# Performance work log

Hardware: AMD Instinct MI355X
Metric: run time of the kernel (lower is better)

Reference implementation:

```python
import jax, jax.numpy as jnp
import numpy as np

N_CLASSES_FG = 20  # n_classes - 1

def _norm(t, axis=1):
    # F.normalize(t, dim=axis, eps=1e-10)
    n = jnp.linalg.norm(t, axis=axis, keepdims=True)
    return t / jnp.maximum(n, 1e-10)

def setup_inputs() -> dict:
    key = jax.random.key(0)
    ks = jax.random.split(key, 6)
    B, C, H, W = 8, 512, 80, 80
    N, Hr, Wr = 100, 40, 40
    return {
        "code_C": jax.random.normal(ks[0], (B, C, H, W), jnp.float32),
        "code_BG": jax.random.normal(ks[1], (B, C, H, W), jnp.float32),
        "ref_code_c": jax.random.normal(ks[2], (N, C, Hr, Wr), jnp.float32),
        "ref_code_bg": jax.random.normal(ks[3], (N, C, Hr, Wr), jnp.float32),
        "sum_patch_coord": jax.random.randint(ks[4], (N, 2), 0, Hr, dtype=jnp.int32),
        "cls_mask": jax.random.randint(ks[5], (N,), 0, N_CLASSES_FG, dtype=jnp.int32),
    }

def reference(code_C, code_BG, ref_code_c, ref_code_bg, sum_patch_coord, cls_mask):
    B, Cdim, H, W = code_C.shape
    N = ref_code_c.shape[0]
    code_C = _norm(code_C)   # channelwise L2 normalize
    code_BG = _norm(code_BG)
    # gather per-annotation feature vectors: ref_code_c[i, :, pc[i,1], pc[i,0]] -> [N, C]
    code_vectors = ref_code_c[jnp.arange(N), :, sum_patch_coord[:, 1], sum_patch_coord[:, 0]]
    # mean-mode prototypes: class-wise mean of gathered vectors
    protos = jax.ops.segment_sum(code_vectors, cls_mask, num_segments=N_CLASSES_FG)  # [V, C]
    counts = jax.ops.segment_sum(jnp.ones((N,), code_vectors.dtype), cls_mask, num_segments=N_CLASSES_FG)
    protos = protos / jnp.maximum(counts, 1.0)[:, None]  # classes with 0 vectors stay zero
    # cosine-similarity maps against normalized prototypes
    prob_C = jnp.einsum('bchw,vc->bvhw', code_C, _norm(protos, axis=1))  # [B, V, H, W]
    # pick the most-background pixel (min of summed class similarity), k=1 topk(-x)
    flat = prob_C.sum(axis=1).reshape(B, -1)  # [B, H*W]
    idx = jnp.argmin(flat, axis=1)
    i_x, i_y = idx // W, idx % W
    min_vec = code_BG[jnp.arange(B), :, i_x, i_y]  # [B, C]
    prob_BG = jnp.einsum('bchw,bc->bhw', code_BG, min_vec)  # [B, H, W]
    probs = jnp.concatenate([prob_BG[:, None], prob_C], axis=1)  # [B, V+1, H, W]
    return jax.nn.softmax(probs, axis=1)
```

## Files before the change

kernel.cpp:

```cpp
#include <hip/hip_runtime.h>
#include <math.h>

#define BB 8
#define CC 512
#define HWSZ 6400
#define NN 100
#define HR 40
#define WR 40
#define VV 20
#define VO 21

__global__ __launch_bounds__(512) void k_protos(const float* __restrict__ refc,
                                                const int* __restrict__ coord,
                                                const int* __restrict__ cls,
                                                float* __restrict__ protosT) {
    const int v = blockIdx.x;
    const int c = threadIdx.x;

    float acc = 0.f;
    int cnt = 0;
    for (int n = 0; n < NN; ++n) {
        if (cls[n] == v) {
            int y = coord[2 * n + 1];
            int x = coord[2 * n + 0];
            acc += refc[((size_t)(n * CC + c) * HR + y) * WR + x];
            ++cnt;
        }
    }
    acc /= fmaxf((float)cnt, 1.0f);

    float ss = acc * acc;
    #pragma unroll
    for (int off = 32; off; off >>= 1) ss += __shfl_xor(ss, off);
    __shared__ float sW[8];
    const int wave = c >> 6, lane = c & 63;
    if (lane == 0) sW[wave] = ss;
    __syncthreads();
    float tot = 0.f;
    #pragma unroll
    for (int w = 0; w < 8; ++w) tot += sW[w];
    float scale = 1.0f / fmaxf(sqrtf(tot), 1e-10f);

    protosT[c * VV + v] = acc * scale;
}

__global__ __launch_bounds__(512, 6) void k_probC(const float* __restrict__ codeC,
                                                  const float* __restrict__ protosT,
                                                  float* __restrict__ probC,
                                                  float* __restrict__ sums) {
    __shared__ float red[8 * VO * 64];
    __shared__ float sScale[64];

    const int tid  = threadIdx.x;
    const int wave = tid >> 6, lane = tid & 63;
    const int b    = blockIdx.x / 100;
    const int tile = blockIdx.x % 100;

    const int c0 = __builtin_amdgcn_readfirstlane(wave * 64);
    const float* src = codeC + ((size_t)(b * CC + c0)) * HWSZ + tile * 64 + lane;
    const float* pt  = protosT + (size_t)c0 * VV;

    float d[VV];
    #pragma unroll
    for (int v = 0; v < VV; ++v) d[v] = 0.f;
    float ss = 0.f;

    #pragma unroll 4
    for (int c = 0; c < 64; ++c) {
        float x = src[(size_t)c * HWSZ];
        ss = fmaf(x, x, ss);
        const float* pr = pt + c * VV;
        #pragma unroll
        for (int v = 0; v < VV; ++v) d[v] = fmaf(x, pr[v], d[v]);
    }

    #pragma unroll
    for (int v = 0; v < VV; ++v) red[(wave * VO + v) * 64 + lane] = d[v];
    red[(wave * VO + VV) * 64 + lane] = ss;
    __syncthreads();

    for (int q = tid; q < VO * 64; q += 512) {
        float t = red[q];
        #pragma unroll
        for (int w = 1; w < 8; ++w) t += red[w * VO * 64 + q];
        red[q] = t;
    }
    __syncthreads();

    if (tid < 64) {
        float ssum = red[VV * 64 + tid];
        sScale[tid] = 1.0f / fmaxf(sqrtf(ssum), 1e-10f);
    }
    __syncthreads();

    float* dst = probC + (size_t)b * VV * HWSZ + tile * 64;
    for (int q = tid; q < VV * 64; q += 512) {
        int v = q >> 6, px = q & 63;
        dst[(size_t)v * HWSZ + px] = red[q] * sScale[px];
    }
    if (tid < 64) {
        float tot = 0.f;
        #pragma unroll
        for (int v = 0; v < VV; ++v) tot += red[v * 64 + tid];
        sums[b * HWSZ + tile * 64 + tid] = tot * sScale[tid];
    }
}

__global__ __launch_bounds__(256) void k_argmin(const float* __restrict__ sums,
                                                const float* __restrict__ codeBG,
                                                float* __restrict__ minvecN) {
    const int b = blockIdx.x;
    const int tid = threadIdx.x;

    float best = INFINITY;
    int bidx = 0x7fffffff;
    for (int p = tid; p < HWSZ; p += 256) {
        float v = sums[b * HWSZ + p];
        if (v < best || (v == best && p < bidx)) { best = v; bidx = p; }
    }
    __shared__ float sV[256];
    __shared__ int   sI[256];
    sV[tid] = best; sI[tid] = bidx;
    __syncthreads();
    for (int off = 128; off; off >>= 1) {
        if (tid < off) {
            float v2 = sV[tid + off]; int i2 = sI[tid + off];
            if (v2 < sV[tid] || (v2 == sV[tid] && i2 < sI[tid])) {
                sV[tid] = v2; sI[tid] = i2;
            }
        }
        __syncthreads();
    }
    const int pix = sI[0];

    __shared__ float sX[CC];
    __shared__ float sR[256];
    float ssp = 0.f;
    for (int c = tid; c < CC; c += 256) {
        float x = codeBG[(size_t)(b * CC + c) * HWSZ + pix];
        sX[c] = x;
        ssp = fmaf(x, x, ssp);
    }
    sR[tid] = ssp;
    __syncthreads();
    for (int off = 128; off; off >>= 1) {
        if (tid < off) sR[tid] += sR[tid + off];
        __syncthreads();
    }
    float scale = 1.0f / fmaxf(sqrtf(sR[0]), 1e-10f);
    for (int c = tid; c < CC; c += 256) minvecN[b * CC + c] = sX[c] * scale;
}

__global__ __launch_bounds__(512, 6) void k_bg_softmax(const float* __restrict__ codeBG,
                                                       const float* __restrict__ minvecN,
                                                       const float* __restrict__ probC,
                                                       float* __restrict__ out) {
    __shared__ float red2[8 * 2 * 64];

    const int tid  = threadIdx.x;
    const int wave = tid >> 6, lane = tid & 63;
    const int b    = blockIdx.x / 100;
    const int tile = blockIdx.x % 100;

    const int c0 = __builtin_amdgcn_readfirstlane(wave * 64);
    const float* src = codeBG + ((size_t)(b * CC + c0)) * HWSZ + tile * 64 + lane;
    const float* mv  = minvecN + b * CC + c0;

    float ss = 0.f, dg = 0.f;
    #pragma unroll 4
    for (int c = 0; c < 64; ++c) {
        float x = src[(size_t)c * HWSZ];
        ss = fmaf(x, x, ss);
        dg = fmaf(x, mv[c], dg);
    }
    red2[(wave * 2 + 0) * 64 + lane] = ss;
    red2[(wave * 2 + 1) * 64 + lane] = dg;
    __syncthreads();

    if (tid < 128) {
        int kind = tid >> 6, px = tid & 63;
        float t = red2[kind * 64 + px];
        #pragma unroll
        for (int w = 1; w < 8; ++w) t += red2[(w * 2 + kind) * 64 + px];
        red2[kind * 64 + px] = t;
    }
    __syncthreads();

    if (tid < 64) {
        const int px = tid;
        float pbg = red2[64 + px] * (1.0f / fmaxf(sqrtf(red2[px]), 1e-10f));

        float pv[VO];
        pv[0] = pbg;
        const float* pc = probC + (size_t)b * VV * HWSZ + tile * 64 + px;
        #pragma unroll
        for (int v = 0; v < VV; ++v) pv[v + 1] = pc[(size_t)v * HWSZ];

        float m = pv[0];
        #pragma unroll
        for (int i = 1; i < VO; ++i) m = fmaxf(m, pv[i]);
        float se = 0.f;
        #pragma unroll
        for (int i = 0; i < VO; ++i) { pv[i] = __expf(pv[i] - m); se += pv[i]; }
        float inv = 1.0f / se;

        float* dst = out + (size_t)b * VO * HWSZ + tile * 64 + px;
        #pragma unroll
        for (int i = 0; i < VO; ++i) dst[(size_t)i * HWSZ] = pv[i] * inv;
    }
}

extern "C" void kernel_launch(void* const* d_in, const int* in_sizes, int n_in,
                              void* d_out, int out_size, void* d_ws, size_t ws_size,
                              hipStream_t stream) {
    const float* codeC  = (const float*)d_in[0];
    const float* codeBG = (const float*)d_in[1];
    const float* refc   = (const float*)d_in[2];
    const int* coord = (const int*)d_in[4];
    const int* cls   = (const int*)d_in[5];
    float* out = (float*)d_out;

    char* ws = (char*)d_ws;
    float* protosT = (float*)(ws);
    float* probC   = (float*)(ws + 40960);
    float* sums    = (float*)(ws + 40960 + 4096000);
    float* minvecN = (float*)(ws + 40960 + 4096000 + 204800);

    k_protos<<<dim3(VV), dim3(512), 0, stream>>>(refc, coord, cls, protosT);
    k_probC<<<dim3(800), dim3(512), 0, stream>>>(codeC, protosT, probC, sums);
    k_argmin<<<dim3(BB), dim3(256), 0, stream>>>(sums, codeBG, minvecN);
    k_bg_softmax<<<dim3(800), dim3(512), 0, stream>>>(codeBG, minvecN, probC, out);
}
```

Measured before the change: 70.67 us.

## Widen pixel tiles, fuse argmin via packed atomicMin, coalesce softmax stores

Both streaming kernels now use 256-thread blocks over 128-pixel tiles. Each thread loads float2 and covers 128 channels, which halves the block count and cross-wave reduction traffic. The per-batch argmin is folded into k_probC: each block packs an order-preserving float key with the pixel index and applies a 64-bit atomicMin. This removes the sums buffer and the separate argmin scan, leaving a small k_minvec kernel. Softmax results are staged in shared memory so all threads write the output, at the cost of fewer blocks (400) and lower occupancy, which may hurt latency hiding.

Result: no change. 71.07 us (+0.6%).

```diff
diff --git a/kernel.cpp b/kernel.cpp
--- a/kernel.cpp
+++ b/kernel.cpp
@@ -9,13 +9,24 @@
 #define WR 40
 #define VV 20
 #define VO 21
+#define TPX 128
+#define NTILE (HWSZ / TPX)
+
+typedef unsigned long long u64;
+
+__device__ __forceinline__ unsigned mapf(float f) {
+    unsigned b = __float_as_uint(f);
+    return (b & 0x80000000u) ? ~b : (b | 0x80000000u);
+}
 
 __global__ __launch_bounds__(512) void k_protos(const float* __restrict__ refc,
                                                 const int* __restrict__ coord,
                                                 const int* __restrict__ cls,
-                                                float* __restrict__ protosT) {
+                                                float* __restrict__ protosT,
+                                                u64* __restrict__ batchMin) {
     const int v = blockIdx.x;
     const int c = threadIdx.x;
+    if (v == 0 && c < BB) batchMin[c] = ~0ull;
 
     float acc = 0.f;
     int cnt = 0;
@@ -44,169 +55,169 @@
     protosT[c * VV + v] = acc * scale;
 }
 
-__global__ __launch_bounds__(512, 6) void k_probC(const float* __restrict__ codeC,
+__global__ __launch_bounds__(256, 2) void k_probC(const float* __restrict__ codeC,
                                                   const float* __restrict__ protosT,
                                                   float* __restrict__ probC,
-                                                  float* __restrict__ sums) {
-    __shared__ float red[8 * VO * 64];
-    __shared__ float sScale[64];
+                                                  u64* __restrict__ batchMin) {
+    __shared__ float red[4 * VO * TPX];
+    __shared__ float sScale[TPX];
+    __shared__ float sPart[2 * TPX];
+    __shared__ u64 sKey[2];
 
     const int tid  = threadIdx.x;
     const int wave = tid >> 6, lane = tid & 63;
-    const int b    = blockIdx.x / 100;
-    const int tile = blockIdx.x % 100;
-
-    const int c0 = __builtin_amdgcn_readfirstlane(wave * 64);
-    const float* src = codeC + ((size_t)(b * CC + c0)) * HWSZ + tile * 64 + lane;
+    const int b    = blockIdx.x / NTILE;
+    const int tile = blockIdx.x % NTILE;
+    const int c0   = __builtin_amdgcn_readfirstlane(wave * 128);
+
+    const float* src = codeC + ((size_t)(b * CC + c0)) * HWSZ + tile * TPX + 2 * lane;
     const float* pt  = protosT + (size_t)c0 * VV;
 
-    float d[VV];
-    #pragma unroll
-    for (int v = 0; v < VV; ++v) d[v] = 0.f;
-    float ss = 0.f;
-
-    #pragma unroll 4
-    for (int c = 0; c < 64; ++c) {
-        float x = src[(size_t)c * HWSZ];
-        ss = fmaf(x, x, ss);
+    float2 d[VV];
+    #pragma unroll
+    for (int v = 0; v < VV; ++v) d[v] = make_float2(0.f, 0.f);
+    float2 ss = make_float2(0.f, 0.f);
+
+    #pragma unroll 8
+    for (int c = 0; c < 128; ++c) {
+        float2 x = *(const float2*)(src + (size_t)c * HWSZ);
+        ss.x = fmaf(x.x, x.x, ss.x);
+        ss.y = fmaf(x.y, x.y, ss.y);
         const float* pr = pt + c * VV;
         #pragma unroll
-        for (int v = 0; v < VV; ++v) d[v] = fmaf(x, pr[v], d[v]);
-    }
-
-    #pragma unroll
-    for (int v = 0; v < VV; ++v) red[(wave * VO + v) * 64 + lane] = d[v];
-    red[(wave * VO + VV) * 64 + lane] = ss;
-    __syncthreads();
-
-    for (int q = tid; q < VO * 64; q += 512) {
-        float t = red[q];
-        #pragma unroll
-        for (int w = 1; w < 8; ++w) t += red[w * VO * 64 + q];
+        for (int v = 0; v < VV; ++v) {
+            float p = pr[v];
+            d[v].x = fmaf(x.x, p, d[v].x);
+            d[v].y = fmaf(x.y, p, d[v].y);
+        }
+    }
+
+    #pragma unroll
+    for (int v = 0; v < VV; ++v) {
+        red[wave * (VO * TPX) + v * TPX + 2 * lane    ] = d[v].x;
+        red[wave * (VO * TPX) + v * TPX + 2 * lane + 1] = d[v].y;
+    }
+    red[wave * (VO * TPX) + VV * TPX + 2 * lane    ] = ss.x;
+    red[wave * (VO * TPX) + VV * TPX + 2 * lane + 1] = ss.y;
+    __syncthreads();
+
+    float psum = 0.f;
+    for (int q = tid; q < VO * TPX; q += 256) {
+        float t = red[q] + red[VO * TPX + q] + red[2 * VO * TPX + q] + red[3 * VO * TPX + q];
         red[q] = t;
-    }
-    __syncthreads();
-
-    if (tid < 64) {
-        float ssum = red[VV * 64 + tid];
-        sScale[tid] = 1.0f / fmaxf(sqrtf(ssum), 1e-10f);
-    }
-    __syncthreads();
-
-    float* dst = probC + (size_t)b * VV * HWSZ + tile * 64;
-    for (int q = tid; q < VV * 64; q += 512) {
-        int v = q >> 6, px = q & 63;
+        if (q < VV * TPX) psum += t;
+    }
+    __syncthreads();
+    if (tid < TPX) sScale[tid] = 1.0f / fmaxf(sqrtf(red[VV * TPX + tid]), 1e-10f);
+    sPart[(tid >> 7) * TPX + (tid & 127)] = psum;
+    __syncthreads();
+
+    float* dst = probC + (size_t)b * VV * HWSZ + tile * TPX;
+    for (int q = tid; q < VV * TPX; q += 256) {
+        int v = q >> 7, px = q & 127;
         dst[(size_t)v * HWSZ + px] = red[q] * sScale[px];
     }
-    if (tid < 64) {
-        float tot = 0.f;
-        #pragma unroll
-        for (int v = 0; v < VV; ++v) tot += red[v * 64 + tid];
-        sums[b * HWSZ + tile * 64 + tid] = tot * sScale[tid];
-    }
-}
-
-__global__ __launch_bounds__(256) void k_argmin(const float* __restrict__ sums,
+
+    if (tid < TPX) {
+        float total = (sPart[tid] + sPart[TPX + tid]) * sScale[tid];
+        u64 key = ((u64)mapf(total) << 32) | (unsigned)(tile * TPX + tid);
+        #pragma unroll
+        for (int off = 32; off; off >>= 1) {
+            u64 o = __shfl_xor(key, off);
+            if (o < key) key = o;
+        }
+        if ((tid & 63) == 0) sKey[tid >> 6] = key;
+    }
+    __syncthreads();
+    if (tid == 0) {
+        u64 k = sKey[0] < sKey[1] ? sKey[0] : sKey[1];
+        atomicMin(&batchMin[b], k);
+    }
+}
+
+__global__ __launch_bounds__(512) void k_minvec(const u64* __restrict__ batchMin,
                                                 const float* __restrict__ codeBG,
                                                 float* __restrict__ minvecN) {
-    const int b = blockIdx.x;
-    const int tid = threadIdx.x;
-
-    float best = INFINITY;
-    int bidx = 0x7fffffff;
-    for (int p = tid; p < HWSZ; p += 256) {
-        float v = sums[b * HWSZ + p];
-        if (v < best || (v == best && p < bidx)) { best = v; bidx = p; }
-    }
-    __shared__ float sV[256];
-    __shared__ int   sI[256];
-    sV[tid] = best; sI[tid] = bidx;
-    __syncthreads();
-    for (int off = 128; off; off >>= 1) {
-        if (tid < off) {
-            float v2 = sV[tid + off]; int i2 = sI[tid + off];
-            if (v2 < sV[tid] || (v2 == sV[tid] && i2 < sI[tid])) {
-                sV[tid] = v2; sI[tid] = i2;
-            }
-        }
-        __syncthreads();
-    }
-    const int pix = sI[0];
-
-    __shared__ float sX[CC];
-    __shared__ float sR[256];
-    float ssp = 0.f;
-    for (int c = tid; c < CC; c += 256) {
-        float x = codeBG[(size_t)(b * CC + c) * HWSZ + pix];
-        sX[c] = x;
-        ssp = fmaf(x, x, ssp);
-    }
-    sR[tid] = ssp;
-    __syncthreads();
-    for (int off = 128; off; off >>= 1) {
-        if (tid < off) sR[tid] += sR[tid + off];
-        __syncthreads();
-    }
-    float scale = 1.0f / fmaxf(sqrtf(sR[0]), 1e-10f);
-    for (int c = tid; c < CC; c += 256) minvecN[b * CC + c] = sX[c] * scale;
-}
-
-__global__ __launch_bounds__(512, 6) void k_bg_softmax(const float* __restrict__ codeBG,
+    const int b = blockIdx.x, c = threadIdx.x;
+    const int pix = (int)(unsigned)(batchMin[b] & 0xFFFFFFFFull);
+    float x = codeBG[(size_t)(b * CC + c) * HWSZ + pix];
+    float ss = x * x;
+    #pragma unroll
+    for (int off = 32; off; off >>= 1) ss += __shfl_xor(ss, off);
+    __shared__ float sW[8];
+    if ((c & 63) == 0) sW[c >> 6] = ss;
+    __syncthreads();
+    float tot = 0.f;
+    #pragma unroll
+    for (int w = 0; w < 8; ++w) tot += sW[w];
+    minvecN[b * CC + c] = x * (1.0f / fmaxf(sqrtf(tot), 1e-10f));
+}
+
+__global__ __launch_bounds__(256, 2) void k_bg_softmax(const float* __restrict__ codeBG,
                                                        const float* __restrict__ minvecN,
                                                        const float* __restrict__ probC,
                                                        float* __restrict__ out) {
-    __shared__ float red2[8 * 2 * 64];
+    __shared__ float red2[4 * 2 * TPX];
+    __shared__ float sExp[VO * TPX];
+    __shared__ float sInv[TPX];
 
     const int tid  = threadIdx.x;
     const int wave = tid >> 6, lane = tid & 63;
-    const int b    = blockIdx.x / 100;
-    const int tile = blockIdx.x % 100;
-
-    const int c0 = __builtin_amdgcn_readfirstlane(wave * 64);
-    const float* src = codeBG + ((size_t)(b * CC + c0)) * HWSZ + tile * 64 + lane;
+    const int b    = blockIdx.x / NTILE;
+    const int tile = blockIdx.x % NTILE;
+    const int c0   = __builtin_amdgcn_readfirstlane(wave * 128);
+
+    const float* src = codeBG + ((size_t)(b * CC + c0)) * HWSZ + tile * TPX + 2 * lane;
     const float* mv  = minvecN + b * CC + c0;
 
-    float ss = 0.f, dg = 0.f;
-    #pragma unroll 4
-    for (int c = 0; c < 64; ++c) {
-        float x = src[(size_t)c * HWSZ];
-        ss = fmaf(x, x, ss);
-        dg = fmaf(x, mv[c], dg);
-    }
-    red2[(wave * 2 + 0) * 64 + lane] = ss;
-    red2[(wave * 2 + 1) * 64 + lane] = dg;
-    __syncthreads();
-
-    if (tid < 128) {
-        int kind = tid >> 6, px = tid & 63;
-        float t = red2[kind * 64 + px];
-        #pragma unroll
-        for (int w = 1; w < 8; ++w) t += red2[(w * 2 + kind) * 64 + px];
-        red2[kind * 64 + px] = t;
-    }
-    __syncthreads();
-
-    if (tid < 64) {
+    float2 ss = make_float2(0.f, 0.f), dg = make_float2(0.f, 0.f);
+    #pragma unroll 8
+    for (int c = 0; c < 128; ++c) {
+        float2 x = *(const float2*)(src + (size_t)c * HWSZ);
+        float m = mv[c];
+        ss.x = fmaf(x.x, x.x, ss.x);
+        ss.y = fmaf(x.y, x.y, ss.y);
+        dg.x = fmaf(x.x, m, dg.x);
+        dg.y = fmaf(x.y, m, dg.y);
+    }
+    red2[wave * (2 * TPX) + 2 * lane    ] = ss.x;
+    red2[wave * (2 * TPX) + 2 * lane + 1] = ss.y;
+    red2[wave * (2 * TPX) + TPX + 2 * lane    ] = dg.x;
+    red2[wave * (2 * TPX) + TPX + 2 * lane + 1] = dg.y;
+    __syncthreads();
+    {
+        int q = tid;
+        float t = red2[q] + red2[2 * TPX + q] + red2[4 * TPX + q] + red2[6 * TPX + q];
+        red2[q] = t;
+    }
+    __syncthreads();
+
+    if (tid < TPX) {
         const int px = tid;
-        float pbg = red2[64 + px] * (1.0f / fmaxf(sqrtf(red2[px]), 1e-10f));
-
+        float pbg = red2[TPX + px] * (1.0f / fmaxf(sqrtf(red2[px]), 1e-10f));
+        const float* pc = probC + (size_t)b * VV * HWSZ + tile * TPX + px;
         float pv[VO];
         pv[0] = pbg;
-        const float* pc = probC + (size_t)b * VV * HWSZ + tile * 64 + px;
         #pragma unroll
         for (int v = 0; v < VV; ++v) pv[v + 1] = pc[(size_t)v * HWSZ];
-
         float m = pv[0];
         #pragma unroll
         for (int i = 1; i < VO; ++i) m = fmaxf(m, pv[i]);
         float se = 0.f;
         #pragma unroll
-        for (int i = 0; i < VO; ++i) { pv[i] = __expf(pv[i] - m); se += pv[i]; }
-        float inv = 1.0f / se;
-
-        float* dst = out + (size_t)b * VO * HWSZ + tile * 64 + px;
-        #pragma unroll
-        for (int i = 0; i < VO; ++i) dst[(size_t)i * HWSZ] = pv[i] * inv;
+        for (int i = 0; i < VO; ++i) {
+            float e = __expf(pv[i] - m);
+            sExp[i * TPX + px] = e;
+            se += e;
+        }
+        sInv[px] = 1.0f / se;
+    }
+    __syncthreads();
+
+    float* dst = out + (size_t)b * VO * HWSZ + tile * TPX;
+    for (int q = tid; q < VO * TPX; q += 256) {
+        int v = q >> 7, px = q & 127;
+        dst[(size_t)v * HWSZ + px] = sExp[q] * sInv[px];
     }
 }
 
@@ -221,13 +232,13 @@
     float* out = (float*)d_out;
 
     char* ws = (char*)d_ws;
-    float* protosT = (float*)(ws);
-    float* probC   = (float*)(ws + 40960);
-    float* sums    = (float*)(ws + 40960 + 4096000);
-    float* minvecN = (float*)(ws + 40960 + 4096000 + 204800);
-
-    k_protos<<<dim3(VV), dim3(512), 0, stream>>>(refc, coord, cls, protosT);
-    k_probC<<<dim3(800), dim3(512), 0, stream>>>(codeC, protosT, probC, sums);
-    k_argmin<<<dim3(BB), dim3(256), 0, stream>>>(sums, codeBG, minvecN);
-    k_bg_softmax<<<dim3(800), dim3(512), 0, stream>>>(codeBG, minvecN, probC, out);
-}
+    float* protosT  = (float*)(ws);
+    float* probC    = (float*)(ws + 40960);
+    float* minvecN  = (float*)(ws + 4136960);
+    u64*   batchMin = (u64*)  (ws + 4153344);
+
+    k_protos    <<<dim3(VV),        dim3(512), 0, stream>>>(refc, coord, cls, protosT, batchMin);
+    k_probC     <<<dim3(BB * NTILE), dim3(256), 0, stream>>>(codeC, protosT, probC, batchMin);
+    k_minvec    <<<dim3(BB),        dim3(512), 0, stream>>>(batchMin, codeBG, minvecN);
+    k_bg_softmax<<<dim3(BB * NTILE), dim3(256), 0, stream>>>(codeBG, minvecN, probC, out);
+}
```
